# Performance work log

Measured on AMD Instinct MI355X. Metric: run time of the kernel, lower is better.

The kernel has to match this reference:

```python
import jax, jax.numpy as jnp
import numpy as np

N = 65536      # total nodes in batched graph
E = 524288     # total edges (avg degree 8)
DIN = 128
DOUT = 128
G = 512        # number of graphs in the batch
NC = 10        # n_class


def _glorot(k, fi, fo):
    lim = np.sqrt(6.0 / (fi + fo)).astype(np.float32)
    return jax.random.uniform(k, (fi, fo), jnp.float32, -lim, lim)


def setup_inputs() -> dict:
    key = jax.random.key(0)
    ks = jax.random.split(key, 16)
    inp = {
        "hx": jax.random.normal(ks[0], (N, DIN), jnp.float32),
        "src": jax.random.randint(ks[1], (E,), 0, N),
        "dst": jax.random.randint(ks[2], (E,), 0, N),
        "graph_id": jnp.sort(jax.random.randint(ks[3], (N,), 0, G)),
        "num_graphs": G,
    }
    dims = [(DIN, DOUT)] + [(DOUT, DOUT)] * 5
    for i, (fi, fo) in enumerate(dims):
        inp[f"W{i+1}"] = _glorot(ks[4 + i], fi, fo)
        inp[f"b{i+1}"] = jnp.zeros((fo,), jnp.float32)
    inp["Wp1"] = _glorot(ks[10], DOUT, DOUT // 2)
    inp["bp1"] = jnp.zeros((DOUT // 2,), jnp.float32)
    inp["Wp2"] = _glorot(ks[11], DOUT // 2, NC)
    inp["bp2"] = jnp.zeros((NC,), jnp.float32)
    return inp


def reference(hx, src, dst, graph_id, num_graphs,
              W1, b1, W2, b2, W3, b3, W4, b4, W5, b5, W6, b6,
              Wp1, bp1, Wp2, bp2):
    n = hx.shape[0]
    ones_e = jnp.ones((src.shape[0],), jnp.float32)
    # DGL GraphConv norm='both': D_out^{-1/2} on src side, D_in^{-1/2} on dst side,
    # degrees clamped to min 1 (allow_zero_in_degree=True).
    deg_out = jax.ops.segment_sum(ones_e, src, num_segments=n)
    deg_in = jax.ops.segment_sum(ones_e, dst, num_segments=n)
    norm_src = jax.lax.rsqrt(jnp.maximum(deg_out, 1.0))[:, None]
    norm_dst = jax.lax.rsqrt(jnp.maximum(deg_in, 1.0))[:, None]

    def gconv(x, W, b):
        m = (x * norm_src)[src]                                  # [E, d] gather
        agg = jax.ops.segment_sum(m, dst, num_segments=n)        # scatter-add
        return (agg * norm_dst) @ W + b

    # 6 stacked conv layers, ReLU; dropout is identity in eval mode
    h = hx
    for W, b in ((W1, b1), (W2, b2), (W3, b3), (W4, b4), (W5, b5), (W6, b6)):
        h = jax.nn.relu(gconv(h, W, b))

    # dgl.mean_nodes: per-graph mean pooling
    pooled = jax.ops.segment_sum(h, graph_id, num_segments=num_graphs)
    cnt = jax.ops.segment_sum(jnp.ones((n,), jnp.float32), graph_id,
                              num_segments=num_graphs)
    pooled = pooled / jnp.maximum(cnt, 1.0)[:, None]

    # pred_lin MLP head
    scores = jax.nn.relu(pooled @ Wp1 + bp1) @ Wp2 + bp2
    # Note: the trailing update_all writes graph.ndata['h'] only (side effect),
    # it does not affect the returned scores, so it is omitted.
    return scores
```

## Files before the change

### kernel.cpp

```cpp
#include <hip/hip_runtime.h>
#include <hip/hip_bf16.h>

#define NN 65536
#define NE 524288
#define DF 128
#define NG 512
#define NCLS 10
#define NBLK 256
#define EPB (NE / NBLK)
#define EPT (EPB / 256)

typedef __bf16 bf16x8 __attribute__((ext_vector_type(8)));
typedef float f32x4 __attribute__((ext_vector_type(4)));
typedef ushort u16x8 __attribute__((ext_vector_type(8)));

__device__ __forceinline__ float bl(uint x) { return __uint_as_float(x << 16); }
__device__ __forceinline__ float bh(uint x) { return __uint_as_float(x & 0xffff0000u); }
__device__ __forceinline__ ushort f2b(float f) {
    uint u = __float_as_uint(f);
    return (ushort)((u + 0x7fffu + ((u >> 16) & 1u)) >> 16);
}


__global__ __launch_bounds__(256) void k_hist(
        const int* __restrict__ src, const int* __restrict__ dst,
        int* __restrict__ Md, int* __restrict__ Ms) {
    __shared__ int hd[256], hs[256];
    int t = threadIdx.x, b = blockIdx.x;
    hd[t] = 0; hs[t] = 0;
    __syncthreads();
    int base = b * EPB;
    for (int k = 0; k < EPT; k++) {
        int e = base + k * 256 + t;
        atomicAdd(&hd[dst[e] >> 8], 1);
        atomicAdd(&hs[src[e] >> 8], 1);
    }
    __syncthreads();
    Md[b * 256 + t] = hd[t];
    Ms[b * 256 + t] = hs[t];
}

__global__ __launch_bounds__(256) void k_colscan(
        const int* __restrict__ Md, const int* __restrict__ Ms,
        int* __restrict__ Bd, int* __restrict__ Bs,
        int* __restrict__ bbd, int* __restrict__ bbs) {
    __shared__ int tot[256];
    int t = threadIdx.x;
    int run = 0;
    for (int b = 0; b < NBLK; b++) { Bd[b * 256 + t] = run; run += Md[b * 256 + t]; }
    tot[t] = run;
    __syncthreads();
    if (t == 0) { int r = 0; for (int i = 0; i < 256; i++) { int c = tot[i]; tot[i] = r; r += c; } }
    __syncthreads();
    bbd[t] = tot[t];
    if (t == 0) bbd[256] = NE;
    __syncthreads();
    run = 0;
    for (int b = 0; b < NBLK; b++) { Bs[b * 256 + t] = run; run += Ms[b * 256 + t]; }
    tot[t] = run;
    __syncthreads();
    if (t == 0) { int r = 0; for (int i = 0; i < 256; i++) { int c = tot[i]; tot[i] = r; r += c; } }
    __syncthreads();
    bbs[t] = tot[t];
    if (t == 0) bbs[256] = NE;
}

__global__ __launch_bounds__(256) void k_place(
        const int* __restrict__ src, const int* __restrict__ dst,
        const int* __restrict__ Bd, const int* __restrict__ bbd,
        const int* __restrict__ Bs, const int* __restrict__ bbs,
        uint* __restrict__ drec, ushort* __restrict__ srec) {
    __shared__ int cd[256], cs[256];
    int t = threadIdx.x, b = blockIdx.x;
    cd[t] = bbd[t] + Bd[b * 256 + t];
    cs[t] = bbs[t] + Bs[b * 256 + t];
    __syncthreads();
    int base = b * EPB;
    for (int k = 0; k < EPT; k++) {
        int e = base + k * 256 + t;
        int d = dst[e], s = src[e];
        int pd = atomicAdd(&cd[d >> 8], 1);
        drec[pd] = ((uint)s << 8) | (uint)(d & 255);
        int ps = atomicAdd(&cs[s >> 8], 1);
        srec[ps] = (ushort)(s & 255);
    }
}

__global__ __launch_bounds__(256) void k_bsort(
        const uint* __restrict__ drec, const int* __restrict__ bbd,
        int* __restrict__ col, int* __restrict__ rp, float* __restrict__ nd) {
    __shared__ int hist[256], cur[256], sc[256];
    __shared__ uint recs[4096];
    __shared__ int colst[4096];
    int t = threadIdx.x, b = blockIdx.x;
    int s0 = bbd[b];
    int n = min(bbd[b + 1] - s0, 4096);
    hist[t] = 0;
    __syncthreads();
    for (int i = t; i < n; i += 256) {
        uint rc = drec[s0 + i];
        recs[i] = rc;
        atomicAdd(&hist[rc & 255u], 1);
    }
    __syncthreads();
    int v = hist[t];
    sc[t] = v;
    __syncthreads();
    for (int off = 1; off < 256; off <<= 1) {
        int x = (t >= off) ? sc[t - off] : 0;
        __syncthreads();
        sc[t] += x;
        __syncthreads();
    }
    int excl = sc[t] - v;
    rp[b * 256 + t] = s0 + excl;
    nd[b * 256 + t] = rsqrtf((float)max(v, 1));
    cur[t] = excl;
    __syncthreads();
    for (int i = t; i < n; i += 256) {
        uint rc = recs[i];
        int p = atomicAdd(&cur[rc & 255u], 1);
        colst[p] = (int)(rc >> 8);
    }
    __syncthreads();
    for (int i = t; i < n; i += 256) col[s0 + i] = colst[i];
    if (b == 0) {
        if (t == 0) rp[NN] = NE;
        if (t < 16) col[NE + t] = 0;
    }
}

__global__ __launch_bounds__(256) void k_shist(
        const ushort* __restrict__ srec, const int* __restrict__ bbs,
        float* __restrict__ ns) {
    __shared__ int hist[256];
    int t = threadIdx.x, b = blockIdx.x;
    hist[t] = 0;
    __syncthreads();
    int s0 = bbs[b], e0 = bbs[b + 1];
    for (int i = s0 + t; i < e0; i += 256)
        atomicAdd(&hist[srec[i] & 255], 1);
    __syncthreads();
    ns[b * 256 + t] = rsqrtf((float)max(hist[t], 1));
}

__global__ void k_scale(const float* __restrict__ hx, const float* __restrict__ ns,
                        uint* __restrict__ xs) {
    int i = blockIdx.x * blockDim.x + threadIdx.x;
    float2 v = ((const float2*)hx)[i];
    float s = ns[i >> 6];
    xs[i] = (uint)f2b(v.x * s) | ((uint)f2b(v.y * s) << 16);
}

__global__ void k_wconv(const float* __restrict__ W, ushort* __restrict__ Wt) {
    int t = blockIdx.x * blockDim.x + threadIdx.x;
    int n = t >> 7, k = t & 127;
    Wt[n * 128 + k] = f2b(W[k * 128 + n]);
}

#define ISSUE(x0, x1, x2, x3, J) { \
    x0 = X32[(size_t)col[(J)] * 64 + lane]; \
    x1 = X32[(size_t)col[(J) + 1] * 64 + lane]; \
    x2 = X32[(size_t)col[(J) + 2] * 64 + lane]; \
    x3 = X32[(size_t)col[(J) + 3] * 64 + lane]; }

#define FLUSHROWS(J) \
    while ((J) >= next_e && r < 15) { \
        Af[r * 132 + 2 * lane] = a0; Af[r * 132 + 2 * lane + 1] = a1; \
        a0 = 0.f; a1 = 0.f; r++; next_e = rp[nb + r + 1]; }

#define PROC1(xv, J) { FLUSHROWS(J) \
    if ((J) < E) { a0 += bl(xv); a1 += bh(xv); } }

__global__ __launch_bounds__(64, 2) void k_fused(
        const uint* __restrict__ X32,
        const int* __restrict__ rp, const int* __restrict__ col,
        const float* __restrict__ nd, const float* __restrict__ ns,
        const uint4* __restrict__ Wg,
        const float* __restrict__ b, int do_scale,
        ushort* __restrict__ out) {
    __shared__ float Af[16 * 132];
    int lane = threadIdx.x;
    int rr = lane & 15;
    int q = lane >> 4;
    int nb = blockIdx.x * 16;

    int S = rp[nb], E = rp[nb + 16];
    int r = 0;
    int next_e = rp[nb + 1];
    float a0 = 0.f, a1 = 0.f;

    uint xa0, xa1, xa2, xa3, xb0, xb1, xb2, xb3;
    uint xc0, xc1, xc2, xc3, xd0, xd1, xd2, xd3;
    int j = S;
    ISSUE(xa0, xa1, xa2, xa3, j)
    ISSUE(xb0, xb1, xb2, xb3, j + 4)
    ISSUE(xc0, xc1, xc2, xc3, j + 8)
    ISSUE(xd0, xd1, xd2, xd3, j + 12)
    for (; j + 16 <= E; j += 16) {
        PROC1(xa0, j)      PROC1(xa1, j + 1)  PROC1(xa2, j + 2)  PROC1(xa3, j + 3)
        ISSUE(xa0, xa1, xa2, xa3, j + 16)
        PROC1(xb0, j + 4)  PROC1(xb1, j + 5)  PROC1(xb2, j + 6)  PROC1(xb3, j + 7)
        ISSUE(xb0, xb1, xb2, xb3, j + 20)
        PROC1(xc0, j + 8)  PROC1(xc1, j + 9)  PROC1(xc2, j + 10) PROC1(xc3, j + 11)
        ISSUE(xc0, xc1, xc2, xc3, j + 24)
        PROC1(xd0, j + 12) PROC1(xd1, j + 13) PROC1(xd2, j + 14) PROC1(xd3, j + 15)
        ISSUE(xd0, xd1, xd2, xd3, j + 28)
    }
    PROC1(xa0, j)      PROC1(xa1, j + 1)  PROC1(xa2, j + 2)  PROC1(xa3, j + 3)
    PROC1(xb0, j + 4)  PROC1(xb1, j + 5)  PROC1(xb2, j + 6)  PROC1(xb3, j + 7)
    PROC1(xc0, j + 8)  PROC1(xc1, j + 9)  PROC1(xc2, j + 10) PROC1(xc3, j + 11)
    PROC1(xd0, j + 12) PROC1(xd1, j + 13) PROC1(xd2, j + 14) PROC1(xd3, j + 15)
    for (; r < 16; r++) {
        Af[r * 132 + 2 * lane] = a0;
        Af[r * 132 + 2 * lane + 1] = a1;
        a0 = 0.f; a1 = 0.f;
    }

    float ndv = nd[nb + rr];
    bf16x8 afr[4];
    #pragma unroll
    for (int ks = 0; ks < 4; ks++) {
        const f32x4* Afv = (const f32x4*)&Af[rr * 132 + ks * 32 + q * 8];
        f32x4 v0 = Afv[0], v1 = Afv[1];
        union { u16x8 u; bf16x8 f; } cv;
        cv.u[0] = f2b(v0[0] * ndv); cv.u[1] = f2b(v0[1] * ndv);
        cv.u[2] = f2b(v0[2] * ndv); cv.u[3] = f2b(v0[3] * ndv);
        cv.u[4] = f2b(v1[0] * ndv); cv.u[5] = f2b(v1[1] * ndv);
        cv.u[6] = f2b(v1[2] * ndv); cv.u[7] = f2b(v1[3] * ndv);
        afr[ks] = cv.f;
    }

    f32x4 cacc[8] = {};
    #pragma unroll
    for (int ks = 0; ks < 4; ks++) {
        #pragma unroll
        for (int ni = 0; ni < 8; ni++) {
            union { uint4 u; bf16x8 f; } bw;
            bw.u = Wg[(size_t)(ni * 16 + rr) * 16 + ks * 4 + q];
            cacc[ni] = __builtin_amdgcn_mfma_f32_16x16x32_bf16(
                afr[ks], bw.f, cacc[ni], 0, 0, 0);
        }
    }

    ushort* Cs = (ushort*)Af;
    float sc4[4];
    #pragma unroll
    for (int rg = 0; rg < 4; rg++)
        sc4[rg] = do_scale ? ns[nb + q * 4 + rg] : 1.f;
    #pragma unroll
    for (int ni = 0; ni < 8; ni++) {
        int c = ni * 16 + rr;
        float bb = b[c];
        #pragma unroll
        for (int rg = 0; rg < 4; rg++) {
            float v = fmaxf(cacc[ni][rg] + bb, 0.f) * sc4[rg];
            Cs[(q * 4 + rg) * 128 + c] = f2b(v);
        }
    }
    const uint4* Cs4 = (const uint4*)Cs;
    uint4* Og = (uint4*)(out + (size_t)nb * 128);
    #pragma unroll
    for (int it = 0; it < 4; it++)
        Og[it * 64 + lane] = Cs4[it * 64 + lane];
}

__global__ void k_gptr(const int* __restrict__ gid, int* __restrict__ gptr) {
    int g = blockIdx.x * blockDim.x + threadIdx.x;
    if (g <= NG) {
        int lo = 0, hi = NN;
        while (lo < hi) {
            int mid = (lo + hi) >> 1;
            if (gid[mid] < g) lo = mid + 1; else hi = mid;
        }
        gptr[g] = lo;
    }
}

__global__ __launch_bounds__(256) void k_pool(
        const uint* __restrict__ h, const int* __restrict__ gptr,
        float* __restrict__ pooled) {
    __shared__ float2 part[256];
    int g = blockIdx.x, t = threadIdx.x;
    int d = t & 63, qq = t >> 6;
    int s = gptr[g], e = gptr[g + 1];
    float2 acc = make_float2(0.f, 0.f);
    for (int i = s + qq; i < e; i += 4) {
        uint x = h[(size_t)i * 64 + d];
        acc.x += bl(x); acc.y += bh(x);
    }
    part[t] = acc;
    __syncthreads();
    if (t < 64) {
        float2 p0 = part[t], p1 = part[t + 64], p2 = part[t + 128], p3 = part[t + 192];
        float inv = 1.f / fmaxf((float)(e - s), 1.f);
        ((float2*)(pooled + g * 128))[t] =
            make_float2((p0.x + p1.x + p2.x + p3.x) * inv,
                        (p0.y + p1.y + p2.y + p3.y) * inv);
    }
}

__global__ __launch_bounds__(64) void k_head(
        const float* __restrict__ pooled,
        const float* __restrict__ Wp1, const float* __restrict__ bp1,
        const float* __restrict__ Wp2, const float* __restrict__ bp2,
        float* __restrict__ scores) {
    __shared__ float p[128];
    __shared__ float t1[64];
    int g = blockIdx.x, t = threadIdx.x;
    p[t] = pooled[g * 128 + t];
    p[t + 64] = pooled[g * 128 + 64 + t];
    __syncthreads();
    float a = 0.f;
    for (int k = 0; k < 128; k++) a += p[k] * Wp1[k * 64 + t];
    t1[t] = fmaxf(a + bp1[t], 0.f);
    __syncthreads();
    if (t < NCLS) {
        float s = bp2[t];
        for (int k = 0; k < 64; k++) s += t1[k] * Wp2[k * NCLS + t];
        scores[g * NCLS + t] = s;
    }
}

extern "C" void kernel_launch(void* const* d_in, const int* in_sizes, int n_in,
                              void* d_out, int out_size, void* d_ws, size_t ws_size,
                              hipStream_t stream) {
    const float* hx  = (const float*)d_in[0];
    const int*   src = (const int*)d_in[1];
    const int*   dst = (const int*)d_in[2];
    const int*   gid = (const int*)d_in[3];
    const float* Ws[6], *bs[6];
    for (int l = 0; l < 6; l++) {
        Ws[l] = (const float*)d_in[5 + 2 * l];
        bs[l] = (const float*)d_in[6 + 2 * l];
    }
    const float* Wp1 = (const float*)d_in[17];
    const float* bp1 = (const float*)d_in[18];
    const float* Wp2 = (const float*)d_in[19];
    const float* bp2 = (const float*)d_in[20];
    float* scores = (float*)d_out;

    char* w = (char*)d_ws;
    ushort* xsA = (ushort*)w;     w += (size_t)NN * DF * 2;
    ushort* xsB = (ushort*)w;     w += (size_t)NN * DF * 2;
    ushort* Wt = (ushort*)w;      w += (size_t)6 * 128 * 128 * 2;
    int* Md   = (int*)w;          w += 256 * 256 * 4;
    int* Ms   = (int*)w;          w += 256 * 256 * 4;
    int* Bd   = (int*)w;          w += 256 * 256 * 4;
    int* Bs   = (int*)w;          w += 256 * 256 * 4;
    int* bbd  = (int*)w;          w += 257 * 4 + 12;
    int* bbs  = (int*)w;          w += 257 * 4 + 12;
    int* rp   = (int*)w;          w += (NN + 1) * 4 + 12;
    int* colv = (int*)w;          w += (NE + 16) * 4;
    float* ns   = (float*)w;      w += NN * 4;
    float* ndst = (float*)w;      w += NN * 4;
    int* gptr   = (int*)w;        w += (NG + 1) * 4 + 12;
    float* pooled = (float*)w;    w += NG * DF * 4;
    uint*   drec = (uint*)xsB;
    ushort* srec = (ushort*)((char*)xsB + (size_t)NE * 4);

    k_hist<<<NBLK, 256, 0, stream>>>(src, dst, Md, Ms);
    k_colscan<<<1, 256, 0, stream>>>(Md, Ms, Bd, Bs, bbd, bbs);
    k_place<<<NBLK, 256, 0, stream>>>(src, dst, Bd, bbd, Bs, bbs, drec, srec);
    k_bsort<<<NBLK, 256, 0, stream>>>(drec, bbd, colv, rp, ndst);
    k_shist<<<NBLK, 256, 0, stream>>>(srec, bbs, ns);
    k_scale<<<NN * 64 / 256, 256, 0, stream>>>(hx, ns, (uint*)xsA);
    for (int l = 0; l < 6; l++)
        k_wconv<<<64, 256, 0, stream>>>(Ws[l], Wt + (size_t)l * 128 * 128);

    ushort* cur = xsA;
    ushort* nxt = xsB;
    for (int l = 0; l < 6; l++) {
        k_fused<<<NN / 16, 64, 0, stream>>>(
            (const uint*)cur, rp, colv, ndst, ns,
            (const uint4*)(Wt + (size_t)l * 128 * 128), bs[l],
            (l < 5) ? 1 : 0, nxt);
        ushort* tmp = cur; cur = nxt; nxt = tmp;
    }

    k_gptr<<<3, 256, 0, stream>>>(gid, gptr);
    k_pool<<<NG, 256, 0, stream>>>((const uint*)cur, gptr, pooled);
    k_head<<<NG, 64, 0, stream>>>(pooled, Wp1, bp1, Wp2, bp2, scores);
}
```

Measured before the change: 294.8 us.

## Load column indices per-lane and broadcast via readlane in aggregation kernel

The fused aggregation kernel now loads 16 column indices at once into lanes, one per lane, and broadcasts each with readlane instead of issuing a scalar or uniform load per edge. It also prefetches the next index chunk a step ahead and caches row pointers in lanes. The column scan is split across two blocks so the dst and src scans run in parallel. The column padding grows to 64 entries to cover the deeper prefetch. The aim is to cut index-load latency and serialization on the gather path, at the cost of extra register pressure and readlane instructions.

```diff
diff --git a/kernel.cpp b/kernel.cpp
--- a/kernel.cpp
+++ b/kernel.cpp
@@ -46,23 +46,18 @@
         int* __restrict__ bbd, int* __restrict__ bbs) {
     __shared__ int tot[256];
     int t = threadIdx.x;
+    const int* M = blockIdx.x ? Ms : Md;
+    int* B = blockIdx.x ? Bs : Bd;
+    int* bb = blockIdx.x ? bbs : bbd;
     int run = 0;
-    for (int b = 0; b < NBLK; b++) { Bd[b * 256 + t] = run; run += Md[b * 256 + t]; }
+    #pragma unroll 8
+    for (int b = 0; b < NBLK; b++) { B[b * 256 + t] = run; run += M[b * 256 + t]; }
     tot[t] = run;
     __syncthreads();
     if (t == 0) { int r = 0; for (int i = 0; i < 256; i++) { int c = tot[i]; tot[i] = r; r += c; } }
     __syncthreads();
-    bbd[t] = tot[t];
-    if (t == 0) bbd[256] = NE;
-    __syncthreads();
-    run = 0;
-    for (int b = 0; b < NBLK; b++) { Bs[b * 256 + t] = run; run += Ms[b * 256 + t]; }
-    tot[t] = run;
-    __syncthreads();
-    if (t == 0) { int r = 0; for (int i = 0; i < 256; i++) { int c = tot[i]; tot[i] = r; r += c; } }
-    __syncthreads();
-    bbs[t] = tot[t];
-    if (t == 0) bbs[256] = NE;
+    bb[t] = tot[t];
+    if (t == 0) bb[256] = NE;
 }
 
 __global__ __launch_bounds__(256) void k_place(
@@ -126,7 +121,7 @@
     for (int i = t; i < n; i += 256) col[s0 + i] = colst[i];
     if (b == 0) {
         if (t == 0) rp[NN] = NE;
-        if (t < 16) col[NE + t] = 0;
+        if (t < 64) col[NE + t] = 0;
     }
 }
 
@@ -158,16 +153,21 @@
     Wt[n * 128 + k] = f2b(W[k * 128 + n]);
 }
 
-#define ISSUE(x0, x1, x2, x3, J) { \
-    x0 = X32[(size_t)col[(J)] * 64 + lane]; \
-    x1 = X32[(size_t)col[(J) + 1] * 64 + lane]; \
-    x2 = X32[(size_t)col[(J) + 2] * 64 + lane]; \
-    x3 = X32[(size_t)col[(J) + 3] * 64 + lane]; }
+#define ISSUE4(x0, x1, x2, x3, CR, K) { \
+    int c0_ = __builtin_amdgcn_readlane((int)(CR), (K)); \
+    int c1_ = __builtin_amdgcn_readlane((int)(CR), (K) + 1); \
+    int c2_ = __builtin_amdgcn_readlane((int)(CR), (K) + 2); \
+    int c3_ = __builtin_amdgcn_readlane((int)(CR), (K) + 3); \
+    x0 = X32[(size_t)c0_ * 64 + lane]; \
+    x1 = X32[(size_t)c1_ * 64 + lane]; \
+    x2 = X32[(size_t)c2_ * 64 + lane]; \
+    x3 = X32[(size_t)c3_ * 64 + lane]; }
 
 #define FLUSHROWS(J) \
     while ((J) >= next_e && r < 15) { \
-        Af[r * 132 + 2 * lane] = a0; Af[r * 132 + 2 * lane + 1] = a1; \
-        a0 = 0.f; a1 = 0.f; r++; next_e = rp[nb + r + 1]; }
+        *(float2*)&Af[r * 132 + 2 * lane] = make_float2(a0, a1); \
+        a0 = 0.f; a1 = 0.f; r++; \
+        next_e = __builtin_amdgcn_readlane(rpv, r + 1); }
 
 #define PROC1(xv, J) { FLUSHROWS(J) \
     if ((J) < E) { a0 += bl(xv); a1 += bh(xv); } }
@@ -185,35 +185,41 @@
     int q = lane >> 4;
     int nb = blockIdx.x * 16;
 
-    int S = rp[nb], E = rp[nb + 16];
+    int rpv = rp[nb + (lane < 16 ? lane : 16)];
+    int S = __builtin_amdgcn_readlane(rpv, 0);
+    int E = __builtin_amdgcn_readlane(rpv, 16);
     int r = 0;
-    int next_e = rp[nb + 1];
+    int next_e = __builtin_amdgcn_readlane(rpv, 1);
     float a0 = 0.f, a1 = 0.f;
+
+    int c0 = col[S + rr];
+    int cA = col[S + 16 + rr];
 
     uint xa0, xa1, xa2, xa3, xb0, xb1, xb2, xb3;
     uint xc0, xc1, xc2, xc3, xd0, xd1, xd2, xd3;
     int j = S;
-    ISSUE(xa0, xa1, xa2, xa3, j)
-    ISSUE(xb0, xb1, xb2, xb3, j + 4)
-    ISSUE(xc0, xc1, xc2, xc3, j + 8)
-    ISSUE(xd0, xd1, xd2, xd3, j + 12)
+    ISSUE4(xa0, xa1, xa2, xa3, c0, 0)
+    ISSUE4(xb0, xb1, xb2, xb3, c0, 4)
+    ISSUE4(xc0, xc1, xc2, xc3, c0, 8)
+    ISSUE4(xd0, xd1, xd2, xd3, c0, 12)
     for (; j + 16 <= E; j += 16) {
+        int cF = col[j + 32 + rr];
         PROC1(xa0, j)      PROC1(xa1, j + 1)  PROC1(xa2, j + 2)  PROC1(xa3, j + 3)
-        ISSUE(xa0, xa1, xa2, xa3, j + 16)
+        ISSUE4(xa0, xa1, xa2, xa3, cA, 0)
         PROC1(xb0, j + 4)  PROC1(xb1, j + 5)  PROC1(xb2, j + 6)  PROC1(xb3, j + 7)
-        ISSUE(xb0, xb1, xb2, xb3, j + 20)
+        ISSUE4(xb0, xb1, xb2, xb3, cA, 4)
         PROC1(xc0, j + 8)  PROC1(xc1, j + 9)  PROC1(xc2, j + 10) PROC1(xc3, j + 11)
-        ISSUE(xc0, xc1, xc2, xc3, j + 24)
+        ISSUE4(xc0, xc1, xc2, xc3, cA, 8)
         PROC1(xd0, j + 12) PROC1(xd1, j + 13) PROC1(xd2, j + 14) PROC1(xd3, j + 15)
-        ISSUE(xd0, xd1, xd2, xd3, j + 28)
+        ISSUE4(xd0, xd1, xd2, xd3, cA, 12)
+        cA = cF;
     }
     PROC1(xa0, j)      PROC1(xa1, j + 1)  PROC1(xa2, j + 2)  PROC1(xa3, j + 3)
     PROC1(xb0, j + 4)  PROC1(xb1, j + 5)  PROC1(xb2, j + 6)  PROC1(xb3, j + 7)
     PROC1(xc0, j + 8)  PROC1(xc1, j + 9)  PROC1(xc2, j + 10) PROC1(xc3, j + 11)
     PROC1(xd0, j + 12) PROC1(xd1, j + 13) PROC1(xd2, j + 14) PROC1(xd3, j + 15)
     for (; r < 16; r++) {
-        Af[r * 132 + 2 * lane] = a0;
-        Af[r * 132 + 2 * lane + 1] = a1;
+        *(float2*)&Af[r * 132 + 2 * lane] = make_float2(a0, a1);
         a0 = 0.f; a1 = 0.f;
     }
 
@@ -351,7 +357,7 @@
     int* bbd  = (int*)w;          w += 257 * 4 + 12;
     int* bbs  = (int*)w;          w += 257 * 4 + 12;
     int* rp   = (int*)w;          w += (NN + 1) * 4 + 12;
-    int* colv = (int*)w;          w += (NE + 16) * 4;
+    int* colv = (int*)w;          w += (NE + 64) * 4;
     float* ns   = (float*)w;      w += NN * 4;
     float* ndst = (float*)w;      w += NN * 4;
     int* gptr   = (int*)w;        w += (NG + 1) * 4 + 12;
@@ -360,7 +366,7 @@
     ushort* srec = (ushort*)((char*)xsB + (size_t)NE * 4);
 
     k_hist<<<NBLK, 256, 0, stream>>>(src, dst, Md, Ms);
-    k_colscan<<<1, 256, 0, stream>>>(Md, Ms, Bd, Bs, bbd, bbs);
+    k_colscan<<<2, 256, 0, stream>>>(Md, Ms, Bd, Bs, bbd, bbs);
     k_place<<<NBLK, 256, 0, stream>>>(src, dst, Bd, bbd, Bs, bbs, drec, srec);
     k_bsort<<<NBLK, 256, 0, stream>>>(drec, bbd, colv, rp, ndst);
     k_shist<<<NBLK, 256, 0, stream>>>(srec, bbs, ns);
```

Result: faster. 285.9 us (-3.0%).
